# Kernel tuning notes

Measured on AMD Instinct MI355X. Metric: run time of the kernel, lower is better.

Reference implementation:

```python
import jax, jax.numpy as jnp
from jax import lax
import numpy as np

P = 7            # patch_size
NP = 10          # n_patches
WIN = 20         # window_size
STRIDE = 4       # window loop stride
EMB = 128        # embedding_dimension
L = WIN - P + 1  # valid-conv output side (14)
HALF = WIN // 2 - P // 2  # window start offset before clipping (7)


def _positions(H, W):
    # x outer, y inner, exactly matching the nested python loops in the source
    return np.array([(x, y) for x in range(0, H - WIN + 1, STRIDE)
                     for y in range(0, W - WIN + 1, STRIDE)], dtype=np.int32)


def _forward(images, Wp, bp, pos_emb, Wb, bb):
    B, C, H, W = images.shape
    BC = B * C
    pos = jnp.asarray(_positions(H, W))  # [Ppos, 2]

    def per_pos(p):
        x, y = p[0], p[1]
        xb0 = jnp.maximum(x - HALF, 0)          # clipped window start (x / cols)
        yb0 = jnp.maximum(y - HALF, 0)          # clipped window start (y / rows)
        winW = jnp.minimum(x - HALF + WIN, W) - xb0  # clipped window width
        winH = jnp.minimum(y - HALF + WIN, H) - yb0  # clipped window height
        # reference patch: rows y:y+P, cols x:x+P (from ORIGINAL data, as in source)
        ref = lax.dynamic_slice(images, (0, 0, y, x), (B, C, P, P)).reshape(BC, 1, P, P)
        # fixed-size window slice; upper bound never clips for our dims, lower-clip
        # handled by masking invalid candidate offsets below
        win = lax.dynamic_slice(images, (0, 0, yb0, xb0), (B, C, WIN, WIN)).reshape(BC, WIN, WIN)
        # grouped cross-correlation == torch conv2d(groups=BC) similarity
        sim = lax.conv_general_dilated(win[None], ref, (1, 1), 'VALID',
                                       feature_group_count=BC,
                                       dimension_numbers=('NCHW', 'OIHW', 'NCHW'))[0]  # [BC,L,L]
        valid = (jnp.arange(L)[:, None] <= winH - P) & (jnp.arange(L)[None, :] <= winW - P)
        sim = jnp.where(valid[None], sim, -jnp.inf)
        _, idx = lax.top_k(sim.reshape(BC, L * L), NP)  # [BC, NP]
        oy, ox = idx // L, idx % L  # row / col offsets inside the window

        def extract(w2, a, b):
            # source's meshgrid indexing yields the TRANSPOSED patch, flattened
            return lax.dynamic_slice(w2, (a, b), (P, P)).T.reshape(P * P)
        patches = jax.vmap(jax.vmap(extract, in_axes=(None, 0, 0)))(win, oy, ox)  # [BC,NP,P*P]
        # source bug kept: x_coords = row offset + x window start (and vice versa)
        return patches, oy + xb0, ox + yb0

    patches, xi, yi = jax.vmap(per_pos)(pos)  # [Ppos,BC,NP,49], [Ppos,BC,NP] int32 x2

    # NOTE: the TransformerEncoder output is discarded in the source; the actual
    # math is back_projection(projection(patches) + pos_emb).
    emb = patches.reshape(-1, B, C, NP, P * P) @ Wp + bp + pos_emb  # [Ppos,B,C,NP,EMB]
    den = (emb @ Wb + bb).reshape(-1, BC, NP, P, P)                 # [Ppos,BC,NP,P,P]

    img0 = images.reshape(BC, H, W)
    cnt0 = jnp.ones((BC, H, W), images.dtype)

    def upd(im, cn, x_i, y_i, d):
        reg = lax.dynamic_slice(im, (y_i, x_i), (P, P))
        c = lax.dynamic_slice(cn, (y_i, x_i), (P, P))
        im = lax.dynamic_update_slice(im, (reg * c + d) / (c + 1.0), (y_i, x_i))
        # source bug kept: counter incremented at transposed slice [x, y]
        ct = lax.dynamic_slice(cn, (x_i, y_i), (P, P)) + 1.0
        cn = lax.dynamic_update_slice(cn, ct, (x_i, y_i))
        return im, cn
    vupd = jax.vmap(upd)  # (b,c) planes are independent -> vectorize

    def n_step(carry, t):
        d, x_i, y_i = t
        return vupd(carry[0], carry[1], x_i, y_i, d), None

    def pos_step(carry, t):
        d, x_i, y_i = t  # d:[BC,NP,P,P]
        carry, _ = lax.scan(n_step, carry, (jnp.moveaxis(d, 1, 0), x_i.T, y_i.T))
        return carry, None

    (img, _), _ = lax.scan(pos_step, (img0, cnt0), (den, xi, yi))
    return img.reshape(B, C, H, W)


def setup_inputs() -> dict:
    key = jax.random.key(0)
    k0, k1, k2, k3 = jax.random.split(key, 4)
    B, C, H, W = 4, 8, 160, 160
    return {
        'images': jax.random.normal(k0, (B, C, H, W), jnp.float32),
        'Wp': jax.random.normal(k1, (P * P, EMB), jnp.float32) * 0.05,
        'bp': jnp.zeros((EMB,), jnp.float32),
        'pos_emb': jax.random.normal(k2, (1, NP, EMB), jnp.float32),
        'Wb': jax.random.normal(k3, (EMB, P * P), jnp.float32) * 0.05,
        'bb': jnp.zeros((P * P,), jnp.float32),
    }


def reference(images, Wp, bp, pos_emb, Wb, bb):
    return _forward(images, Wp, bp, pos_emb, Wb, bb)
```

## Files before the change

### kernel.cpp

```cpp
#include <hip/hip_runtime.h>

#define PS 7
#define NP 10
#define WIN 20
#define STR 4
#define LL 14
#define HALF 7
#define HH 160
#define WW 160
#define BCN 32
#define NX 36
#define PPOS 1296
#define EMBD 128
#define NTASK (BCN * PPOS * NP)
#define NEV (PPOS * NP)
#define CAP 512
#define NTILE 400

__global__ __launch_bounds__(256) void k_mk(const float* __restrict__ Wp,
                                            const float* __restrict__ bp,
                                            const float* __restrict__ pe,
                                            const float* __restrict__ Wb,
                                            const float* __restrict__ bb,
                                            float* __restrict__ M,
                                            float* __restrict__ K) {
    int t = blockIdx.x * 256 + threadIdx.x;
    if (t < 49 * 49) {
        int k = t / 49, d = t % 49;
        float acc = 0.f;
        for (int e = 0; e < EMBD; ++e) acc += Wp[k * EMBD + e] * Wb[e * 49 + d];
        M[t] = acc;
    } else if (t < 49 * 49 + NP * 49) {
        int u = t - 49 * 49;
        int n = u / 49, d = u % 49;
        float acc = bb[d];
        for (int e = 0; e < EMBD; ++e) acc += (bp[e] + pe[n * EMBD + e]) * Wb[e * 49 + d];
        K[u] = acc;
    }
}

__global__ __launch_bounds__(256) void k_sim(const float* __restrict__ img,
                                             const float* __restrict__ Mg,
                                             const float* __restrict__ Kg,
                                             unsigned* __restrict__ xy,
                                             float* __restrict__ pd) {
    int tid  = threadIdx.x;
    int wv   = __builtin_amdgcn_readfirstlane(tid >> 6);
    int lane = tid & 63;
    int gt   = blockIdx.x * 4 + wv;
    int pos  = gt % PPOS;
    int bc   = gt / PPOS;
    int ix = pos / NX, iy = pos % NX;
    int x = ix * STR, y = iy * STR;
    int xb0 = max(x - HALF, 0), yb0 = max(y - HALF, 0);
    int jmax = x + 6 - xb0;
    int imax = y + 6 - yb0;
    const float* plane = img + bc * (HH * WW);

    float rf[49];
#pragma unroll
    for (int a = 0; a < PS; ++a)
#pragma unroll
        for (int b = 0; b < PS; ++b)
            rf[a * 7 + b] = plane[(y + a) * WW + (x + b)];

    int B = lane;
    bool bval = B < 56;
    int gr = B / 14, c = B % 14;
    int r0 = gr * 4;
    float acc[4] = {0.f, 0.f, 0.f, 0.f};
    const float* wb = plane + yb0 * WW + xb0 + c;
#pragma unroll
    for (int a = 0; a < 10; ++a) {
        int ra = min(r0 + a, 19);
        const float* rp = wb + ra * WW;
#pragma unroll
        for (int b = 0; b < 7; ++b) {
            float tap = rp[b];
#pragma unroll
            for (int k = 0; k < 4; ++k) {
                int ai = a - k;
                if (ai >= 0 && ai < 7) acc[k] += tap * rf[ai * 7 + b];
            }
        }
    }
    float v[4]; int vidx[4];
#pragma unroll
    for (int k = 0; k < 4; ++k) {
        int rr = r0 + k;
        bool ok = bval && (rr <= imax) && (c <= jmax);
        v[k] = ok ? acc[k] : -INFINITY;
        vidx[k] = rr * 14 + c;
    }

    int ld = min(lane, 48);
    float Mc[49];
#pragma unroll
    for (int j = 0; j < 49; ++j) Mc[j] = Mg[j * 49 + ld];

    bool act = lane < 49;
    int tbase = (bc * PPOS + pos) * NP;

    for (int n = 0; n < NP; ++n) {
        float bv = fmaxf(fmaxf(v[0], v[1]), fmaxf(v[2], v[3]));
#pragma unroll
        for (int off = 32; off >= 1; off >>= 1)
            bv = fmaxf(bv, __shfl_xor(bv, off));
        unsigned long long ms[4];
        ms[0] = __ballot(v[0] == bv);
        ms[1] = __ballot(v[1] == bv);
        ms[2] = __ballot(v[2] == bv);
        ms[3] = __ballot(v[3] == bv);
        int best = 1 << 30, slotw = 0, lanew = 0;
#pragma unroll
        for (int s = 0; s < 4; ++s) {
            if (ms[s]) {
                int l  = __ffsll(ms[s]) - 1;
                int id = __builtin_amdgcn_readlane(vidx[s], l);
                if (id < best) { best = id; slotw = s; lanew = l; }
            }
        }
        int bi = best;
#pragma unroll
        for (int s = 0; s < 4; ++s)
            if (s == slotw && lane == lanew) v[s] = -INFINITY;

        int oy = bi / 14, ox = bi % 14;
        int x_i = oy + xb0;
        int y_i = ox + yb0;
        int t = tbase + n;
        if (lane == 0) xy[t] = (unsigned)x_i | ((unsigned)y_i << 8);
        const float* src = plane + (yb0 + oy) * WW + (xb0 + ox);
        float den = Kg[n * 49 + ld];
#pragma unroll
        for (int j = 0; j < 49; ++j)
            den = fmaf(src[(j % 7) * WW + (j / 7)], Mc[j], den);
        if (act) pd[(size_t)t * 49 + lane] = den;
    }
}

__global__ __launch_bounds__(256) void k_apply(const float* __restrict__ img,
                                               const unsigned* __restrict__ xy,
                                               const float* __restrict__ pd,
                                               float* __restrict__ out) {
    __shared__ unsigned lsts[4][CAP];
    int tid  = threadIdx.x;
    int wv   = tid >> 6;
    int lane = tid & 63;
    int gt   = blockIdx.x * 4 + wv;
    int bc   = gt / NTILE;
    int tile = gt % NTILE;
    int tx0 = (tile % 20) * 8, ty0 = (tile / 20) * 8;
    int tx1 = tx0 + 7, ty1 = ty0 + 7;
    const unsigned* xs = xy + bc * NEV;
    unsigned* lst = lsts[wv];

    int a0 = (tx0 <= 19) ? 0 : ((tx0 - 9) >> 2), a1 = min(35, (tx0 + 14) >> 2);
    int b0 = (ty0 <= 19) ? 0 : ((ty0 - 9) >> 2), b1 = min(35, (ty0 + 14) >> 2);
    if (a0 > b0) { int t0 = a0; a0 = b0; b0 = t0; int t1 = a1; a1 = b1; b1 = t1; }
    int lo0 = a0, lo1 = 0, len0, len1;
    if (b0 <= a1 + 1) { len0 = max(a1, b1) - lo0 + 1; len1 = 0; }
    else              { len0 = a1 - a0 + 1; lo1 = b0; len1 = b1 - b0 + 1; }
    int nU = len0 + len1;
    unsigned m = 65536u / (unsigned)nU + 1u;
    int npos = nU * nU;

    unsigned cnt = 0;
    for (int base = 0; base < npos; base += 64) {
        int k = base + lane;
        bool valid = k < npos;
        unsigned kk = valid ? (unsigned)k : 0u;
        int ki = (int)((kk * m) >> 16);
        int kj = (int)kk - ki * nU;
        int ixp = (ki < len0) ? (lo0 + ki) : (lo1 + ki - len0);
        int iyp = (kj < len0) ? (lo0 + kj) : (lo1 + kj - len0);
        int pos = ixp * NX + iyp;
        const unsigned* ep = xs + pos * NP;

        unsigned ev[NP];
#pragma unroll
        for (int n = 0; n < NP; ++n) ev[n] = ep[n];

        unsigned rel = 0;
        unsigned pk[NP];
#pragma unroll
        for (int n = 0; n < NP; ++n) {
            unsigned u = ev[n];
            int x_i = (int)(u & 255u);
            int y_i = (int)((u >> 8) & 255u);
            bool ih = (x_i <= tx1) && (x_i + 6 >= tx0) &&
                      (y_i <= ty1) && (y_i + 6 >= ty0);
            bool ch = (x_i <= ty1) && (x_i + 6 >= ty0) &&
                      (y_i <= tx1) && (y_i + 6 >= tx0);
            bool any = valid && (ih || ch);
            rel |= any ? (1u << n) : 0u;
            pk[n] = (unsigned)(pos * NP + n) | ((unsigned)x_i << 14) | ((unsigned)y_i << 22)
                  | (ih ? (1u << 30) : 0u) | (ch ? (1u << 31) : 0u);
        }
        int myc = __popc(rel);
        int scan = myc;
#pragma unroll
        for (int off = 1; off < 64; off <<= 1) {
            int o = __shfl_up(scan, off);
            scan += (lane >= off) ? o : 0;
        }
        int excl  = (int)cnt + scan - myc;
        int total = __shfl(scan, 63);
        int w = excl;
#pragma unroll
        for (int n = 0; n < NP; ++n) {
            if ((rel >> n) & 1u) { if (w < CAP) lst[w] = pk[n]; ++w; }
        }
        cnt += (unsigned)total;
    }
    if (cnt > CAP) cnt = CAP;
    unsigned cntp = (cnt + 7u) & ~7u;
    if (cntp > CAP) cntp = CAP;
    if (lane < (int)(cntp - cnt)) lst[cnt + lane] = 0u;
    int cntN = (int)cntp;

    int r  = ty0 + (lane >> 3);
    int cc = tx0 + (lane & 7);
    float im = img[bc * (HH * WW) + r * WW + cc];
    float c  = 1.0f;
    const float* ds = pd + (size_t)bc * ((size_t)NEV * 49);
    int vOff = (r * 7 + cc) * 4;

    for (int i = 0; i < cntN; i += 8) {
        unsigned eu[8];
        float    dv[8];
#pragma unroll
        for (int j = 0; j < 8; ++j)
            eu[j] = (unsigned)__builtin_amdgcn_readfirstlane((int)lst[i + j]);
#pragma unroll
        for (int j = 0; j < 8; ++j) {
            unsigned u = eu[j];
            int t    = (int)(u & 16383u);
            int x_i  = (int)((u >> 14) & 255u);
            int y_i  = (int)((u >> 22) & 255u);
            int sOff = (y_i * 7 + x_i) * 4;
            const char* dsb = (const char*)(ds + (size_t)t * 49);
            int boc = min(max(vOff - sOff, 0), 192);
            dv[j] = *(const float*)(dsb + boc);
        }
#pragma unroll
        for (int j = 0; j < 8; ++j) {
            unsigned u = eu[j];
            int x_i = (int)((u >> 14) & 255u);
            int y_i = (int)((u >> 22) & 255u);
            int dr = r - y_i, dc = cc - x_i;
            bool h = (u & (1u << 30)) && (((unsigned)dr <= 6u) & ((unsigned)dc <= 6u));
            float nim = fmaf(im, c, dv[j]) * __builtin_amdgcn_rcpf(c + 1.0f);
            im = h ? nim : im;
            int er = r - x_i, ec = cc - y_i;
            bool hc = (u >> 31) && (((unsigned)er <= 6u) & ((unsigned)ec <= 6u));
            c += hc ? 1.0f : 0.0f;
        }
    }
    out[bc * (HH * WW) + r * WW + cc] = im;
}

extern "C" void kernel_launch(void* const* d_in, const int* in_sizes, int n_in,
                              void* d_out, int out_size, void* d_ws, size_t ws_size,
                              hipStream_t stream) {
    const float* img = (const float*)d_in[0];
    const float* Wp  = (const float*)d_in[1];
    const float* bp  = (const float*)d_in[2];
    const float* pe  = (const float*)d_in[3];
    const float* Wb  = (const float*)d_in[4];
    const float* bb  = (const float*)d_in[5];
    float* out = (float*)d_out;

    float* wsf = (float*)d_ws;
    float*    M   = wsf;
    float*    K   = wsf + 2404;
    unsigned* xy  = (unsigned*)(wsf + 2896);
    float*    pd  = wsf + 2896 + NTASK;

    k_mk<<<12, 256, 0, stream>>>(Wp, bp, pe, Wb, bb, M, K);
    k_sim<<<BCN * PPOS / 4, 256, 0, stream>>>(img, M, K, xy, pd);
    k_apply<<<BCN * NTILE / 4, 256, 0, stream>>>(img, xy, pd, out);
}
```

Measured before the change: 295.7 us.

## Use precomputed 8x8 tile hit-masks as wave masks and split den FMA chain

k_mk now also builds a 256-entry table of 64-bit lane masks giving which pixels of an 8x8 tile a 7x7 patch at each relative offset covers. In k_apply each list entry becomes a uint2 carrying tile-relative mask indices and a precomputed pd byte offset, and the per-lane hit tests are replaced by v_cndmask with the scalar mask loaded from the table. k_sim splits the 49-term dot product into four independent accumulators to shorten the dependency chain. The cost is double-width LDS list entries, extra scalar loads of mask words, inline asm, and a slightly different float summation order.

```diff
diff --git a/kernel.cpp b/kernel.cpp
--- a/kernel.cpp
+++ b/kernel.cpp
@@ -23,7 +23,8 @@
                                             const float* __restrict__ Wb,
                                             const float* __restrict__ bb,
                                             float* __restrict__ M,
-                                            float* __restrict__ K) {
+                                            float* __restrict__ K,
+                                            unsigned long long* __restrict__ MT) {
     int t = blockIdx.x * 256 + threadIdx.x;
     if (t < 49 * 49) {
         int k = t / 49, d = t % 49;
@@ -36,6 +37,18 @@
         float acc = bb[d];
         for (int e = 0; e < EMBD; ++e) acc += (bp[e] + pe[n * EMBD + e]) * Wb[e * 49 + d];
         K[u] = acc;
+    } else if (t < 49 * 49 + NP * 49 + 256) {
+        int u = t - (49 * 49 + NP * 49);
+        int ey = (u >> 4) - 7, ex = (u & 15) - 7;
+        int r0 = ey > 0 ? ey : 0, r1 = ey + 6 < 7 ? ey + 6 : 7;
+        int c0 = ex > 0 ? ex : 0, c1 = ex + 6 < 7 ? ex + 6 : 7;
+        unsigned long long m = 0ull;
+        if (r0 <= r1 && c0 <= c1) {
+            unsigned colp = ((1u << (c1 - c0 + 1)) - 1u) << c0;
+            for (int rr = r0; rr <= r1; ++rr)
+                m |= (unsigned long long)colp << (8 * rr);
+        }
+        MT[u] = m;
     }
 }
 
@@ -131,10 +144,16 @@
         int t = tbase + n;
         if (lane == 0) xy[t] = (unsigned)x_i | ((unsigned)y_i << 8);
         const float* src = plane + (yb0 + oy) * WW + (xb0 + ox);
-        float den = Kg[n * 49 + ld];
-#pragma unroll
-        for (int j = 0; j < 49; ++j)
-            den = fmaf(src[(j % 7) * WW + (j / 7)], Mc[j], den);
+        float d0 = Kg[n * 49 + ld], d1 = 0.f, d2 = 0.f, d3 = 0.f;
+#pragma unroll
+        for (int j = 0; j < 48; j += 4) {
+            d0 = fmaf(src[((j + 0) % 7) * WW + ((j + 0) / 7)], Mc[j + 0], d0);
+            d1 = fmaf(src[((j + 1) % 7) * WW + ((j + 1) / 7)], Mc[j + 1], d1);
+            d2 = fmaf(src[((j + 2) % 7) * WW + ((j + 2) / 7)], Mc[j + 2], d2);
+            d3 = fmaf(src[((j + 3) % 7) * WW + ((j + 3) / 7)], Mc[j + 3], d3);
+        }
+        d0 = fmaf(src[(48 % 7) * WW + (48 / 7)], Mc[48], d0);
+        float den = (d0 + d1) + (d2 + d3);
         if (act) pd[(size_t)t * 49 + lane] = den;
     }
 }
@@ -142,8 +161,9 @@
 __global__ __launch_bounds__(256) void k_apply(const float* __restrict__ img,
                                                const unsigned* __restrict__ xy,
                                                const float* __restrict__ pd,
+                                               const unsigned long long* __restrict__ mt,
                                                float* __restrict__ out) {
-    __shared__ unsigned lsts[4][CAP];
+    __shared__ uint2 lsts[4][CAP];
     int tid  = threadIdx.x;
     int wv   = tid >> 6;
     int lane = tid & 63;
@@ -153,7 +173,7 @@
     int tx0 = (tile % 20) * 8, ty0 = (tile / 20) * 8;
     int tx1 = tx0 + 7, ty1 = ty0 + 7;
     const unsigned* xs = xy + bc * NEV;
-    unsigned* lst = lsts[wv];
+    uint2* lst = lsts[wv];
 
     int a0 = (tx0 <= 19) ? 0 : ((tx0 - 9) >> 2), a1 = min(35, (tx0 + 14) >> 2);
     int b0 = (ty0 <= 19) ? 0 : ((ty0 - 9) >> 2), b1 = min(35, (ty0 + 14) >> 2);
@@ -182,7 +202,7 @@
         for (int n = 0; n < NP; ++n) ev[n] = ep[n];
 
         unsigned rel = 0;
-        unsigned pk[NP];
+        unsigned w0[NP], w1[NP];
 #pragma unroll
         for (int n = 0; n < NP; ++n) {
             unsigned u = ev[n];
@@ -194,8 +214,13 @@
                       (y_i <= tx1) && (y_i + 6 >= tx0);
             bool any = valid && (ih || ch);
             rel |= any ? (1u << n) : 0u;
-            pk[n] = (unsigned)(pos * NP + n) | ((unsigned)x_i << 14) | ((unsigned)y_i << 22)
-                  | (ih ? (1u << 30) : 0u) | (ch ? (1u << 31) : 0u);
+            int eyH = y_i - ty0, exH = x_i - tx0;
+            int eyC = x_i - ty0, exC = y_i - tx0;
+            unsigned hidx = ih ? (unsigned)(((eyH + 7) << 4) | (exH + 7)) : 0u;
+            unsigned cidx = ch ? (unsigned)(((eyC + 7) << 4) | (exC + 7)) : 0u;
+            unsigned s8q  = ih ? (unsigned)(((7 * eyH + exH) + 48) << 2) : 0u;
+            w0[n] = (unsigned)(pos * NP + n);
+            w1[n] = hidx | (cidx << 8) | (s8q << 16);
         }
         int myc = __popc(rel);
         int scan = myc;
@@ -209,52 +234,53 @@
         int w = excl;
 #pragma unroll
         for (int n = 0; n < NP; ++n) {
-            if ((rel >> n) & 1u) { if (w < CAP) lst[w] = pk[n]; ++w; }
+            if ((rel >> n) & 1u) { if (w < CAP) lst[w] = make_uint2(w0[n], w1[n]); ++w; }
         }
         cnt += (unsigned)total;
     }
     if (cnt > CAP) cnt = CAP;
     unsigned cntp = (cnt + 7u) & ~7u;
     if (cntp > CAP) cntp = CAP;
-    if (lane < (int)(cntp - cnt)) lst[cnt + lane] = 0u;
+    if (lane < (int)(cntp - cnt)) lst[cnt + lane] = make_uint2(0u, 0u);
     int cntN = (int)cntp;
 
-    int r  = ty0 + (lane >> 3);
-    int cc = tx0 + (lane & 7);
+    int r8 = lane >> 3, c8 = lane & 7;
+    int r  = ty0 + r8;
+    int cc = tx0 + c8;
     float im = img[bc * (HH * WW) + r * WW + cc];
     float c  = 1.0f;
     const float* ds = pd + (size_t)bc * ((size_t)NEV * 49);
-    int vOff = (r * 7 + cc) * 4;
+    int vOff2 = (r8 * 7 + c8) * 4 + 192;
 
     for (int i = 0; i < cntN; i += 8) {
-        unsigned eu[8];
+        unsigned u0[8], u1[8];
         float    dv[8];
 #pragma unroll
-        for (int j = 0; j < 8; ++j)
-            eu[j] = (unsigned)__builtin_amdgcn_readfirstlane((int)lst[i + j]);
-#pragma unroll
         for (int j = 0; j < 8; ++j) {
-            unsigned u = eu[j];
-            int t    = (int)(u & 16383u);
-            int x_i  = (int)((u >> 14) & 255u);
-            int y_i  = (int)((u >> 22) & 255u);
-            int sOff = (y_i * 7 + x_i) * 4;
+            uint2 e = lst[i + j];
+            u0[j] = (unsigned)__builtin_amdgcn_readfirstlane((int)e.x);
+            u1[j] = (unsigned)__builtin_amdgcn_readfirstlane((int)e.y);
+        }
+#pragma unroll
+        for (int j = 0; j < 8; ++j) {
+            int t = (int)u0[j];
             const char* dsb = (const char*)(ds + (size_t)t * 49);
-            int boc = min(max(vOff - sOff, 0), 192);
+            int boc = min(max(vOff2 - (int)((u1[j] >> 16) & 511u), 0), 192);
             dv[j] = *(const float*)(dsb + boc);
         }
+        unsigned long long hmv[8], cmv[8];
 #pragma unroll
         for (int j = 0; j < 8; ++j) {
-            unsigned u = eu[j];
-            int x_i = (int)((u >> 14) & 255u);
-            int y_i = (int)((u >> 22) & 255u);
-            int dr = r - y_i, dc = cc - x_i;
-            bool h = (u & (1u << 30)) && (((unsigned)dr <= 6u) & ((unsigned)dc <= 6u));
+            hmv[j] = mt[u1[j] & 255u];
+            cmv[j] = mt[(u1[j] >> 8) & 255u];
+        }
+#pragma unroll
+        for (int j = 0; j < 8; ++j) {
             float nim = fmaf(im, c, dv[j]) * __builtin_amdgcn_rcpf(c + 1.0f);
-            im = h ? nim : im;
-            int er = r - x_i, ec = cc - y_i;
-            bool hc = (u >> 31) && (((unsigned)er <= 6u) & ((unsigned)ec <= 6u));
-            c += hc ? 1.0f : 0.0f;
+            asm("v_cndmask_b32 %0, %0, %1, %2" : "+v"(im) : "v"(nim), "s"(hmv[j]));
+            float inc;
+            asm("v_cndmask_b32 %0, 0, 1.0, %1" : "=v"(inc) : "s"(cmv[j]));
+            c += inc;
         }
     }
     out[bc * (HH * WW) + r * WW + cc] = im;
@@ -272,12 +298,13 @@
     float* out = (float*)d_out;
 
     float* wsf = (float*)d_ws;
-    float*    M   = wsf;
-    float*    K   = wsf + 2404;
-    unsigned* xy  = (unsigned*)(wsf + 2896);
-    float*    pd  = wsf + 2896 + NTASK;
-
-    k_mk<<<12, 256, 0, stream>>>(Wp, bp, pe, Wb, bb, M, K);
+    float*              M  = wsf;
+    float*              K  = wsf + 2404;
+    unsigned long long* MT = (unsigned long long*)(wsf + 2896);
+    unsigned*           xy = (unsigned*)(wsf + 3408);
+    float*              pd = wsf + 3408 + NTASK;
+
+    k_mk<<<13, 256, 0, stream>>>(Wp, bp, pe, Wb, bb, M, K, MT);
     k_sim<<<BCN * PPOS / 4, 256, 0, stream>>>(img, M, K, xy, pd);
-    k_apply<<<BCN * NTILE / 4, 256, 0, stream>>>(img, xy, pd, out);
+    k_apply<<<BCN * NTILE / 4, 256, 0, stream>>>(img, xy, pd, MT, out);
 }
```

Result: faster. 283.2 us (-4.2%).
